# Optimization experiments

Measured on AMD Instinct MI355X. Metric: run time of the kernel, lower is better.

The kernel has to match this reference:

```python
import jax, jax.numpy as jnp
import numpy as np

B, S, DIM_VAL, DIM_ATTN = 8, 2048, 512, 512

def setup_inputs() -> dict:
    key = jax.random.key(0)
    k1, k2, k3, k4 = jax.random.split(key, 4)
    x = jax.random.normal(k1, (B, S, DIM_VAL), dtype=jnp.float32)
    # nn.Linear weights are [out_features, in_features], no bias
    scale = 1.0 / np.sqrt(DIM_VAL)
    Wq = jax.random.uniform(k2, (DIM_ATTN, DIM_VAL), dtype=jnp.float32, minval=-scale, maxval=scale)
    Wk = jax.random.uniform(k3, (DIM_ATTN, DIM_VAL), dtype=jnp.float32, minval=-scale, maxval=scale)
    Wv = jax.random.uniform(k4, (DIM_VAL, DIM_VAL), dtype=jnp.float32, minval=-scale, maxval=scale)
    return {"x": x, "Wq": Wq, "Wk": Wk, "Wv": Wv}

def reference(x, Wq, Wk, Wv):
    # Q,K: [B,S,dim_attn]; V: [B,S,dim_val]
    Q = jnp.einsum('bsd,ad->bsa', x, Wq)
    K = jnp.einsum('bsd,ad->bsa', x, Wk)
    V = jnp.einsum('bsd,vd->bsv', x, Wv)
    scores = jnp.einsum('bqa,bka->bqk', Q, K) / jnp.sqrt(jnp.asarray(Q.shape[-1], dtype=Q.dtype))
    attn = jax.nn.softmax(scores, axis=-1)
    return jnp.einsum('bqk,bkv->bqv', attn, V)
```

## Files before the change

### kernel.cpp

```cpp
#include <hip/hip_runtime.h>
#include <hip/hip_bf16.h>
#include <math.h>

#define BQ   8
#define SEQ  2048
#define DV   512
#define DA   512
#define MTOT (BQ * SEQ)

typedef __attribute__((ext_vector_type(8))) short bf16x8;
typedef __attribute__((ext_vector_type(4))) float f32x4;
typedef __attribute__((ext_vector_type(4))) short short4v;

__device__ __forceinline__ unsigned short f2bf(float f) {
    union { float f; unsigned u; } c; c.f = f;
    unsigned u = c.u;
    unsigned r = (u + 0x7fffu + ((u >> 16) & 1u)) >> 16;
    return (unsigned short)r;
}
__device__ __forceinline__ float bf2f(unsigned short h) {
    union { unsigned u; float f; } c; c.u = ((unsigned)h) << 16;
    return c.f;
}

__device__ __forceinline__ void gload_lds16(const void* g, void* l) {
    __builtin_amdgcn_global_load_lds(
        (const __attribute__((address_space(1))) void*)g,
        (__attribute__((address_space(3))) void*)l,
        16, 0, 0);
}

__global__ __launch_bounds__(256) void cvt_f32_bf16(
    const float* __restrict__ in, short* __restrict__ out, int n4)
{
    int i = blockIdx.x * blockDim.x + threadIdx.x;
    int stride = gridDim.x * blockDim.x;
    for (; i < n4; i += stride) {
        float4 v = ((const float4*)in)[i];
        short4v o;
        o[0] = (short)f2bf(v.x);
        o[1] = (short)f2bf(v.y);
        o[2] = (short)f2bf(v.z);
        o[3] = (short)f2bf(v.w);
        ((short4v*)out)[i] = o;
    }
}

template<int OMODE>
__global__ __launch_bounds__(256, 2) void gemm_bt(
    const short* __restrict__ A, const short* __restrict__ B, void* __restrict__ Cv,
    int M, int N, int K, int lda, int ldb, int ldc,
    long strideA, long strideB, long strideC, float scale)
{
    __shared__ __align__(16) short sA[128 * 32];
    __shared__ __align__(16) short sB[128 * 32];

    const int tid  = threadIdx.x;
    const int wave = tid >> 6;
    const int lane = tid & 63;
    const int wr = wave >> 1, wc = wave & 1;
    const int brow = blockIdx.y * 128;
    const int bcol = blockIdx.x * 128;
    const int z = blockIdx.z;
    A += (size_t)z * strideA;
    B += (size_t)z * strideB;

    const int r16 = lane & 15;
    const int kq  = lane >> 4;

    f32x4 acc[4][4];
    const f32x4 fz = {0.f, 0.f, 0.f, 0.f};
    #pragma unroll
    for (int i = 0; i < 4; ++i)
        #pragma unroll
        for (int j = 0; j < 4; ++j) acc[i][j] = fz;

    for (int k0 = 0; k0 < K; k0 += 32) {
        #pragma unroll
        for (int j = 0; j < 2; ++j) {
            int slot = wave * 128 + j * 64 + lane;
            int row  = slot >> 2;
            int cs   = slot & 3;
            const short* ga = A + (size_t)(brow + row) * lda + k0 + cs * 8;
            const short* gb = B + (size_t)(bcol + row) * ldb + k0 + cs * 8;
            int ldsoff = (wave * 128 + j * 64) * 8;
            gload_lds16(ga, &sA[ldsoff]);
            gload_lds16(gb, &sB[ldsoff]);
        }
        __syncthreads();

        bf16x8 a[4], b[4];
        #pragma unroll
        for (int i = 0; i < 4; ++i)
            a[i] = *(const bf16x8*)&sA[(wr * 64 + i * 16 + r16) * 32 + kq * 8];
        #pragma unroll
        for (int j = 0; j < 4; ++j)
            b[j] = *(const bf16x8*)&sB[(wc * 64 + j * 16 + r16) * 32 + kq * 8];

        #pragma unroll
        for (int i = 0; i < 4; ++i)
            #pragma unroll
            for (int j = 0; j < 4; ++j)
                acc[i][j] = __builtin_amdgcn_mfma_f32_16x16x32_bf16(a[i], b[j], acc[i][j], 0, 0, 0);
        __syncthreads();
    }

    #pragma unroll
    for (int i = 0; i < 4; ++i) {
        int row0 = brow + wr * 64 + i * 16 + (lane >> 4) * 4;
        #pragma unroll
        for (int j = 0; j < 4; ++j) {
            int col = bcol + wc * 64 + j * 16 + (lane & 15);
            f32x4 v = acc[i][j];
            #pragma unroll
            for (int t = 0; t < 4; ++t) {
                float val = v[t] * scale;
                int row = row0 + t;
                if (OMODE == 0) {
                    ((short*)Cv)[(size_t)z * strideC + (size_t)row * ldc + col] = (short)f2bf(val);
                } else if (OMODE == 1) {
                    ((float*)Cv)[(size_t)z * strideC + (size_t)row * ldc + col] = val;
                } else {
                    int bb = row >> 11;
                    int s  = row & (SEQ - 1);
                    ((short*)Cv)[(size_t)bb * ((size_t)N * SEQ) + (size_t)col * SEQ + s] = (short)f2bf(val);
                }
            }
        }
    }
}

__global__ __launch_bounds__(256) void softmax_rows(short* __restrict__ S)
{
    int row  = blockIdx.x * 4 + (threadIdx.x >> 6);
    int lane = threadIdx.x & 63;
    size_t base = (size_t)row * SEQ;

    float v[32];
    #pragma unroll
    for (int c = 0; c < 4; ++c) {
        bf16x8 x = *(const bf16x8*)&S[base + c * 512 + lane * 8];
        #pragma unroll
        for (int e = 0; e < 8; ++e) v[c * 8 + e] = bf2f((unsigned short)x[e]);
    }
    float mx = -1e30f;
    #pragma unroll
    for (int i = 0; i < 32; ++i) mx = fmaxf(mx, v[i]);
    #pragma unroll
    for (int off = 32; off > 0; off >>= 1) mx = fmaxf(mx, __shfl_xor(mx, off));

    float sum = 0.f;
    #pragma unroll
    for (int i = 0; i < 32; ++i) { v[i] = __expf(v[i] - mx); sum += v[i]; }
    #pragma unroll
    for (int off = 32; off > 0; off >>= 1) sum += __shfl_xor(sum, off);
    float inv = 1.0f / sum;

    #pragma unroll
    for (int c = 0; c < 4; ++c) {
        bf16x8 x;
        #pragma unroll
        for (int e = 0; e < 8; ++e) x[e] = (short)f2bf(v[c * 8 + e] * inv);
        *(bf16x8*)&S[base + c * 512 + lane * 8] = x;
    }
}

extern "C" void kernel_launch(void* const* d_in, const int* in_sizes, int n_in,
                              void* d_out, int out_size, void* d_ws, size_t ws_size,
                              hipStream_t stream)
{
    const float* x  = (const float*)d_in[0];
    const float* Wq = (const float*)d_in[1];
    const float* Wk = (const float*)d_in[2];
    const float* Wv = (const float*)d_in[3];
    float* out = (float*)d_out;

    short* xb  = (short*)d_ws;
    short* wqb = xb  + (size_t)MTOT * DV;
    short* wkb = wqb + (size_t)DA * DV;
    short* wvb = wkb + (size_t)DA * DV;
    short* Qb  = wvb + (size_t)DV * DV;
    short* Kb  = Qb  + (size_t)MTOT * DA;
    short* VT  = Kb  + (size_t)MTOT * DA;
    short* Sc  = VT  + (size_t)MTOT * DV;

    const float qscale = 0.04419417382415922f;

    cvt_f32_bf16<<<8192, 256, 0, stream>>>(x,  xb,  (MTOT * DV) / 4);
    cvt_f32_bf16<<<256,  256, 0, stream>>>(Wq, wqb, (DA * DV) / 4);
    cvt_f32_bf16<<<256,  256, 0, stream>>>(Wk, wkb, (DA * DV) / 4);
    cvt_f32_bf16<<<256,  256, 0, stream>>>(Wv, wvb, (DV * DV) / 4);

    dim3 blk(256);

    gemm_bt<0><<<dim3(4, 128, 1), blk, 0, stream>>>(
        xb, wqb, Qb, MTOT, DA, DV, DV, DV, DA, 0, 0, 0, qscale);
    gemm_bt<0><<<dim3(4, 128, 1), blk, 0, stream>>>(
        xb, wkb, Kb, MTOT, DA, DV, DV, DV, DA, 0, 0, 0, 1.0f);
    gemm_bt<2><<<dim3(4, 128, 1), blk, 0, stream>>>(
        xb, wvb, VT, MTOT, DV, DV, DV, DV, SEQ, 0, 0, 0, 1.0f);

    gemm_bt<0><<<dim3(16, 16, BQ), blk, 0, stream>>>(
        Qb, Kb, Sc, SEQ, SEQ, DA, DA, DA, SEQ,
        (long)SEQ * DA, (long)SEQ * DA, (long)SEQ * SEQ, 1.0f);

    softmax_rows<<<(BQ * SEQ) / 4, 256, 0, stream>>>(Sc);

    gemm_bt<1><<<dim3(4, 16, BQ), blk, 0, stream>>>(
        Sc, VT, out, SEQ, DV, SEQ, SEQ, SEQ, DV,
        (long)SEQ * SEQ, (long)DV * SEQ, (long)SEQ * DV, 1.0f);
}
```

Baseline: 276.1 us.

## Replace 128x128 GEMM with pipelined 256x256 swizzled-LDS kernel and fuse QKV projections

Replaces the simple 128x128 bf16 MFMA GEMM with a 512-thread, 256x256-tile kernel. It double-buffers 64-wide K slices in 128 KB of dynamic LDS with XOR-swizzled layout, interleaves async global-to-LDS loads with MFMA quarters using explicit barriers, waitcnts and setprio, and remaps workgroups across XCDs. The three Q/K/V projection GEMMs are fused into one launch over the contiguous concatenated weights, with the epilogue routing columns to Q (scaled), K, or transposed V. The goal is more data reuse per tile and overlap of loads with compute. The risks are lower occupancy and too few blocks for the PV GEMM (128 workgroups), plus reliance on the weight buffers being adjacent.

```diff
diff --git a/kernel.cpp b/kernel.cpp
--- a/kernel.cpp
+++ b/kernel.cpp
@@ -28,6 +28,12 @@
         (const __attribute__((address_space(1))) void*)g,
         (__attribute__((address_space(3))) void*)l,
         16, 0, 0);
+}
+
+__device__ __forceinline__ void barx() {
+    __builtin_amdgcn_sched_barrier(0);
+    __builtin_amdgcn_s_barrier();
+    __builtin_amdgcn_sched_barrier(0);
 }
 
 __global__ __launch_bounds__(256) void cvt_f32_bf16(
@@ -47,83 +53,195 @@
 }
 
 template<int OMODE>
-__global__ __launch_bounds__(256, 2) void gemm_bt(
+__global__ __launch_bounds__(512, 2) void gemm256(
     const short* __restrict__ A, const short* __restrict__ B, void* __restrict__ Cv,
-    int M, int N, int K, int lda, int ldb, int ldc,
+    int ntx, int K, int lda, int ldb, int ldc,
     long strideA, long strideB, long strideC, float scale)
 {
-    __shared__ __align__(16) short sA[128 * 32];
-    __shared__ __align__(16) short sB[128 * 32];
+    extern __shared__ short lds[];
+    short* const bufA0 = lds;
+    short* const bufA1 = lds + 16384;
+    short* const bufB0 = lds + 32768;
+    short* const bufB1 = lds + 49152;
 
     const int tid  = threadIdx.x;
-    const int wave = tid >> 6;
     const int lane = tid & 63;
-    const int wr = wave >> 1, wc = wave & 1;
-    const int brow = blockIdx.y * 128;
-    const int bcol = blockIdx.x * 128;
+    const int wv   = tid >> 6;
+    const int wr   = wv >> 2;
+    const int wc   = wv & 3;
+    const int r16  = lane & 15;
+    const int kq   = lane >> 4;
+    const int swz  = (r16 & 7) * 8;
+    const int cs[2] = { (kq * 8) ^ swz, (32 + kq * 8) ^ swz };
+    const int aOff = (wr * 128 + r16) * 64;
+    const int bOff = (wc * 64  + r16) * 64;
+
+    const int nwg = gridDim.x;
+    const int wg  = blockIdx.x;
+    const int q8  = nwg >> 3, r8 = nwg & 7;
+    const int xcd = wg & 7, off8 = wg >> 3;
+    const int swg = (xcd < r8 ? xcd * (q8 + 1) : r8 * (q8 + 1) + (xcd - r8) * q8) + off8;
+    const int tx = swg % ntx, ty = swg / ntx;
+    const int brow = ty * 256, bcol = tx * 256;
     const int z = blockIdx.z;
-    A += (size_t)z * strideA;
-    B += (size_t)z * strideB;
-
-    const int r16 = lane & 15;
-    const int kq  = lane >> 4;
-
-    f32x4 acc[4][4];
+
+    A += (size_t)z * strideA + (size_t)brow * lda;
+    B += (size_t)z * strideB + (size_t)bcol * ldb;
+
+    auto stageHalf = [&](const short* gbase, int ld, short* region, int h) {
+        #pragma unroll
+        for (int c = 0; c < 2; ++c) {
+            int s    = h * 1024 + c * 512 + tid;
+            int row  = s >> 3;
+            int chnk = (s & 7) ^ (row & 7);
+            gload_lds16(gbase + (size_t)row * ld + chnk * 8, region + s * 8);
+        }
+    };
+
+    f32x4 acc[8][4];
     const f32x4 fz = {0.f, 0.f, 0.f, 0.f};
     #pragma unroll
-    for (int i = 0; i < 4; ++i)
+    for (int i = 0; i < 8; ++i)
         #pragma unroll
         for (int j = 0; j < 4; ++j) acc[i][j] = fz;
 
-    for (int k0 = 0; k0 < K; k0 += 32) {
-        #pragma unroll
-        for (int j = 0; j < 2; ++j) {
-            int slot = wave * 128 + j * 64 + lane;
-            int row  = slot >> 2;
-            int cs   = slot & 3;
-            const short* ga = A + (size_t)(brow + row) * lda + k0 + cs * 8;
-            const short* gb = B + (size_t)(bcol + row) * ldb + k0 + cs * 8;
-            int ldsoff = (wave * 128 + j * 64) * 8;
-            gload_lds16(ga, &sA[ldsoff]);
-            gload_lds16(gb, &sB[ldsoff]);
-        }
-        __syncthreads();
-
-        bf16x8 a[4], b[4];
-        #pragma unroll
-        for (int i = 0; i < 4; ++i)
-            a[i] = *(const bf16x8*)&sA[(wr * 64 + i * 16 + r16) * 32 + kq * 8];
-        #pragma unroll
-        for (int j = 0; j < 4; ++j)
-            b[j] = *(const bf16x8*)&sB[(wc * 64 + j * 16 + r16) * 32 + kq * 8];
-
+    bf16x8 af[4][2], bfr[4][2];
+
+    auto dsA = [&](const short* base, int ibase) {
         #pragma unroll
         for (int i = 0; i < 4; ++i)
             #pragma unroll
-            for (int j = 0; j < 4; ++j)
-                acc[i][j] = __builtin_amdgcn_mfma_f32_16x16x32_bf16(a[i], b[j], acc[i][j], 0, 0, 0);
-        __syncthreads();
-    }
-
-    #pragma unroll
-    for (int i = 0; i < 4; ++i) {
-        int row0 = brow + wr * 64 + i * 16 + (lane >> 4) * 4;
+            for (int kk = 0; kk < 2; ++kk)
+                af[i][kk] = *(const bf16x8*)(base + aOff + (ibase + i) * 1024 + cs[kk]);
+    };
+    auto dsB = [&](const short* base, int jbase) {
+        #pragma unroll
+        for (int j = 0; j < 2; ++j)
+            #pragma unroll
+            for (int kk = 0; kk < 2; ++kk)
+                bfr[jbase + j][kk] = *(const bf16x8*)(base + bOff + (jbase + j) * 1024 + cs[kk]);
+    };
+    auto doQ = [&](int ibase, int jbase) {
+        __builtin_amdgcn_s_setprio(1);
+        #pragma unroll
+        for (int i = 0; i < 4; ++i)
+            #pragma unroll
+            for (int j = 0; j < 2; ++j)
+                #pragma unroll
+                for (int kk = 0; kk < 2; ++kk)
+                    acc[ibase + i][jbase + j] = __builtin_amdgcn_mfma_f32_16x16x32_bf16(
+                        af[i][kk], bfr[jbase + j][kk], acc[ibase + i][jbase + j], 0, 0, 0);
+        __builtin_amdgcn_s_setprio(0);
+    };
+
+    const int NT = K >> 6;
+
+    stageHalf(B,      ldb, bufB0, 0);  stageHalf(B,      ldb, bufB0, 1);
+    stageHalf(A,      lda, bufA0, 0);  stageHalf(A,      lda, bufA0, 1);
+    stageHalf(B + 64, ldb, bufB1, 0);  stageHalf(B + 64, ldb, bufB1, 1);
+    asm volatile("s_waitcnt vmcnt(4)" ::: "memory");
+    barx();
+
+    for (int t = 0; t < NT; t += 2) {
+        const bool s2 = (t + 2) < NT;
+        const bool s3 = (t + 3) < NT;
+        const short* At1 = A + (t + 1) * 64;
+        const short* At2 = A + (t + 2) * 64;
+        const short* Bt2 = B + (t + 2) * 64;
+        const short* Bt3 = B + (t + 3) * 64;
+
+        dsA(bufA0, 0); dsB(bufB0, 0);
+        stageHalf(At1, lda, bufA1, 0);
+        barx();
+        asm volatile("s_waitcnt lgkmcnt(0)" ::: "memory");
+        __builtin_amdgcn_sched_barrier(0);
+        doQ(0, 0);
+        barx();
+
+        dsB(bufB0, 2);
+        stageHalf(At1, lda, bufA1, 1);
+        barx();
+        asm volatile("s_waitcnt lgkmcnt(0)" ::: "memory");
+        __builtin_amdgcn_sched_barrier(0);
+        doQ(0, 2);
+        barx();
+
+        dsA(bufA0, 4);
+        if (s2) stageHalf(Bt2, ldb, bufB0, 0);
+        barx();
+        asm volatile("s_waitcnt lgkmcnt(0)" ::: "memory");
+        __builtin_amdgcn_sched_barrier(0);
+        doQ(4, 0);
+        barx();
+
+        if (s2) stageHalf(Bt2, ldb, bufB0, 1);
+        if (s2) asm volatile("s_waitcnt vmcnt(4)" ::: "memory");
+        else    asm volatile("s_waitcnt vmcnt(0)" ::: "memory");
+        barx();
+        doQ(4, 2);
+        barx();
+
+        dsA(bufA1, 0); dsB(bufB1, 0);
+        if (s2) stageHalf(At2, lda, bufA0, 0);
+        barx();
+        asm volatile("s_waitcnt lgkmcnt(0)" ::: "memory");
+        __builtin_amdgcn_sched_barrier(0);
+        doQ(0, 0);
+        barx();
+
+        dsB(bufB1, 2);
+        if (s2) stageHalf(At2, lda, bufA0, 1);
+        barx();
+        asm volatile("s_waitcnt lgkmcnt(0)" ::: "memory");
+        __builtin_amdgcn_sched_barrier(0);
+        doQ(0, 2);
+        barx();
+
+        dsA(bufA1, 4);
+        if (s3) stageHalf(Bt3, ldb, bufB1, 0);
+        barx();
+        asm volatile("s_waitcnt lgkmcnt(0)" ::: "memory");
+        __builtin_amdgcn_sched_barrier(0);
+        doQ(4, 0);
+        barx();
+
+        if (s3) stageHalf(Bt3, ldb, bufB1, 1);
+        if (s3) asm volatile("s_waitcnt vmcnt(4)" ::: "memory");
+        else    asm volatile("s_waitcnt vmcnt(0)" ::: "memory");
+        barx();
+        doQ(4, 2);
+        barx();
+    }
+
+    const int orow = (lane >> 4) * 4;
+    #pragma unroll
+    for (int i = 0; i < 8; ++i) {
+        int grow = brow + wr * 128 + i * 16 + orow;
         #pragma unroll
         for (int j = 0; j < 4; ++j) {
-            int col = bcol + wc * 64 + j * 16 + (lane & 15);
+            int gcol = bcol + wc * 64 + j * 16 + r16;
             f32x4 v = acc[i][j];
             #pragma unroll
-            for (int t = 0; t < 4; ++t) {
-                float val = v[t] * scale;
-                int row = row0 + t;
+            for (int tt = 0; tt < 4; ++tt) {
+                int row = grow + tt;
                 if (OMODE == 0) {
-                    ((short*)Cv)[(size_t)z * strideC + (size_t)row * ldc + col] = (short)f2bf(val);
+                    ((short*)Cv)[(size_t)z * strideC + (size_t)row * ldc + gcol] =
+                        (short)f2bf(v[tt] * scale);
                 } else if (OMODE == 1) {
-                    ((float*)Cv)[(size_t)z * strideC + (size_t)row * ldc + col] = val;
+                    ((float*)Cv)[(size_t)z * strideC + (size_t)row * ldc + gcol] = v[tt];
                 } else {
-                    int bb = row >> 11;
-                    int s  = row & (SEQ - 1);
-                    ((short*)Cv)[(size_t)bb * ((size_t)N * SEQ) + (size_t)col * SEQ + s] = (short)f2bf(val);
+                    short* Qb = (short*)Cv;
+                    short* Kb = Qb + (size_t)MTOT * DA;
+                    short* VT = Kb + (size_t)MTOT * DA;
+                    if (gcol < 512) {
+                        Qb[(size_t)row * DA + gcol] = (short)f2bf(v[tt] * scale);
+                    } else if (gcol < 1024) {
+                        Kb[(size_t)row * DA + (gcol - 512)] = (short)f2bf(v[tt]);
+                    } else {
+                        int vcol = gcol - 1024;
+                        int bb = row >> 11, ss = row & (SEQ - 1);
+                        VT[((size_t)bb * DV + vcol) * SEQ + ss] = (short)f2bf(v[tt]);
+                    }
                 }
             }
         }
@@ -191,22 +309,23 @@
     cvt_f32_bf16<<<256,  256, 0, stream>>>(Wk, wkb, (DA * DV) / 4);
     cvt_f32_bf16<<<256,  256, 0, stream>>>(Wv, wvb, (DV * DV) / 4);
 
-    dim3 blk(256);
-
-    gemm_bt<0><<<dim3(4, 128, 1), blk, 0, stream>>>(
-        xb, wqb, Qb, MTOT, DA, DV, DV, DV, DA, 0, 0, 0, qscale);
-    gemm_bt<0><<<dim3(4, 128, 1), blk, 0, stream>>>(
-        xb, wkb, Kb, MTOT, DA, DV, DV, DV, DA, 0, 0, 0, 1.0f);
-    gemm_bt<2><<<dim3(4, 128, 1), blk, 0, stream>>>(
-        xb, wvb, VT, MTOT, DV, DV, DV, DV, SEQ, 0, 0, 0, 1.0f);
-
-    gemm_bt<0><<<dim3(16, 16, BQ), blk, 0, stream>>>(
-        Qb, Kb, Sc, SEQ, SEQ, DA, DA, DA, SEQ,
+    hipFuncSetAttribute(reinterpret_cast<const void*>(&gemm256<3>),
+                        hipFuncAttributeMaxDynamicSharedMemorySize, 131072);
+    hipFuncSetAttribute(reinterpret_cast<const void*>(&gemm256<0>),
+                        hipFuncAttributeMaxDynamicSharedMemorySize, 131072);
+    hipFuncSetAttribute(reinterpret_cast<const void*>(&gemm256<1>),
+                        hipFuncAttributeMaxDynamicSharedMemorySize, 131072);
+
+    gemm256<3><<<dim3(6 * 64, 1, 1), 512, 131072, stream>>>(
+        xb, wqb, Qb, 6, DV, DV, DV, 0, 0, 0, 0, qscale);
+
+    gemm256<0><<<dim3(8 * 8, 1, BQ), 512, 131072, stream>>>(
+        Qb, Kb, Sc, 8, DA, DA, DA, SEQ,
         (long)SEQ * DA, (long)SEQ * DA, (long)SEQ * SEQ, 1.0f);
 
     softmax_rows<<<(BQ * SEQ) / 4, 256, 0, stream>>>(Sc);
 
-    gemm_bt<1><<<dim3(4, 16, BQ), blk, 0, stream>>>(
-        Sc, VT, out, SEQ, DV, SEQ, SEQ, SEQ, DV,
+    gemm256<1><<<dim3(2 * 8, 1, BQ), 512, 131072, stream>>>(
+        Sc, VT, out, 2, SEQ, SEQ, SEQ, DV,
         (long)SEQ * SEQ, (long)DV * SEQ, (long)SEQ * DV, 1.0f);
 }
```

New measurement: 279.1 us. About the same (+1.1%).

## Fuse Q/K/V projections into one GEMM and swizzle LDS tile layout

Applied to the files above, without the earlier changes.

The three projection GEMMs become a single launch over a concatenated 1536-wide weight (wq, wk, wv stored contiguously in the workspace), and an output mode routes each column range to Q (scaled), K, or transposed V. The LDS chunk index is XOR-swizzled by row on both store and load to reduce bank conflicts on the MFMA operand reads. This cuts kernel launches, reads x from memory once for all three projections, and uses a larger grid. The epilogue gains per-element branching, and the fused GEMM depends on the weight buffers being adjacent in memory.

```diff
diff --git a/kernel.cpp b/kernel.cpp
--- a/kernel.cpp
+++ b/kernel.cpp
@@ -67,6 +67,7 @@
 
     const int r16 = lane & 15;
     const int kq  = lane >> 4;
+    const int csw = (kq ^ (r16 & 3)) * 8;
 
     f32x4 acc[4][4];
     const f32x4 fz = {0.f, 0.f, 0.f, 0.f};
@@ -80,7 +81,7 @@
         for (int j = 0; j < 2; ++j) {
             int slot = wave * 128 + j * 64 + lane;
             int row  = slot >> 2;
-            int cs   = slot & 3;
+            int cs   = (slot & 3) ^ (row & 3);
             const short* ga = A + (size_t)(brow + row) * lda + k0 + cs * 8;
             const short* gb = B + (size_t)(bcol + row) * ldb + k0 + cs * 8;
             int ldsoff = (wave * 128 + j * 64) * 8;
@@ -92,10 +93,10 @@
         bf16x8 a[4], b[4];
         #pragma unroll
         for (int i = 0; i < 4; ++i)
-            a[i] = *(const bf16x8*)&sA[(wr * 64 + i * 16 + r16) * 32 + kq * 8];
+            a[i] = *(const bf16x8*)&sA[(wr * 64 + i * 16 + r16) * 32 + csw];
         #pragma unroll
         for (int j = 0; j < 4; ++j)
-            b[j] = *(const bf16x8*)&sB[(wc * 64 + j * 16 + r16) * 32 + kq * 8];
+            b[j] = *(const bf16x8*)&sB[(wc * 64 + j * 16 + r16) * 32 + csw];
 
         #pragma unroll
         for (int i = 0; i < 4; ++i)
@@ -114,16 +115,26 @@
             f32x4 v = acc[i][j];
             #pragma unroll
             for (int t = 0; t < 4; ++t) {
-                float val = v[t] * scale;
                 int row = row0 + t;
                 if (OMODE == 0) {
-                    ((short*)Cv)[(size_t)z * strideC + (size_t)row * ldc + col] = (short)f2bf(val);
+                    ((short*)Cv)[(size_t)z * strideC + (size_t)row * ldc + col] =
+                        (short)f2bf(v[t] * scale);
                 } else if (OMODE == 1) {
-                    ((float*)Cv)[(size_t)z * strideC + (size_t)row * ldc + col] = val;
+                    ((float*)Cv)[(size_t)z * strideC + (size_t)row * ldc + col] = v[t];
                 } else {
-                    int bb = row >> 11;
-                    int s  = row & (SEQ - 1);
-                    ((short*)Cv)[(size_t)bb * ((size_t)N * SEQ) + (size_t)col * SEQ + s] = (short)f2bf(val);
+                    short* Qb = (short*)Cv;
+                    short* Kb = Qb + (size_t)MTOT * DA;
+                    short* VT = Kb + (size_t)MTOT * DA;
+                    if (col < 512) {
+                        Qb[(size_t)row * DA + col] = (short)f2bf(v[t] * scale);
+                    } else if (col < 1024) {
+                        Kb[(size_t)row * DA + (col - 512)] = (short)f2bf(v[t]);
+                    } else {
+                        int vcol = col - 1024;
+                        int bb = row >> 11;
+                        int ss = row & (SEQ - 1);
+                        VT[((size_t)bb * DV + vcol) * SEQ + ss] = (short)f2bf(v[t]);
+                    }
                 }
             }
         }
@@ -193,12 +204,8 @@
 
     dim3 blk(256);
 
-    gemm_bt<0><<<dim3(4, 128, 1), blk, 0, stream>>>(
-        xb, wqb, Qb, MTOT, DA, DV, DV, DV, DA, 0, 0, 0, qscale);
-    gemm_bt<0><<<dim3(4, 128, 1), blk, 0, stream>>>(
-        xb, wkb, Kb, MTOT, DA, DV, DV, DV, DA, 0, 0, 0, 1.0f);
-    gemm_bt<2><<<dim3(4, 128, 1), blk, 0, stream>>>(
-        xb, wvb, VT, MTOT, DV, DV, DV, DV, SEQ, 0, 0, 0, 1.0f);
+    gemm_bt<3><<<dim3(12, 128, 1), blk, 0, stream>>>(
+        xb, wqb, Qb, MTOT, 1536, DV, DV, DV, 0, 0, 0, 0, qscale);
 
     gemm_bt<0><<<dim3(16, 16, BQ), blk, 0, stream>>>(
         Qb, Kb, Sc, SEQ, SEQ, DA, DA, DA, SEQ,
```

Result: no change. 281.4 us (+1.9%).
